# Performance work log

Measured on AMD Instinct MI355X. Metric: run time of the kernel, lower is better.

The kernel has to match this reference:

```python
import jax, jax.numpy as jnp
import numpy as np

NEG_FILL = -1e4  # finite stand-in for -inf so sort/cumsum stay NaN-free


def entmax15(X):
    """1.5-entmax along the last axis (Peters et al. 2019, sort-based exact algorithm)."""
    X = X - jnp.max(X, axis=-1, keepdims=True)
    X = X * 0.5  # alpha=1.5 transform
    Xsrt = -jnp.sort(-X, axis=-1)  # descending sort
    S = X.shape[-1]
    rho = jnp.arange(1, S + 1, dtype=X.dtype)  # 1..S support-size candidates
    mean = jnp.cumsum(Xsrt, axis=-1) / rho
    mean_sq = jnp.cumsum(Xsrt * Xsrt, axis=-1) / rho
    ss = rho * (mean_sq - mean * mean)          # running k*variance
    delta = (1.0 - ss) / rho
    tau = mean - jnp.sqrt(jnp.clip(delta, 0.0, None))
    support_size = jnp.sum(tau <= Xsrt, axis=-1, keepdims=True)
    tau_star = jnp.take_along_axis(tau, support_size - 1, axis=-1)
    return jnp.square(jnp.clip(X - tau_star, 0.0, None))


def setup_inputs() -> dict:
    key = jax.random.key(0)
    k1, k2 = jax.random.split(key)
    B, S = 32768, 2048
    scores = jax.random.normal(k1, (B, S), dtype=jnp.float32)
    mask = jax.random.randint(k2, (B, S), 0, 2, dtype=jnp.int32)
    mask = mask.at[:, 0].set(1)  # guarantee at least one unmasked token per row
    return {"scores": scores, "mask": mask}


def reference(scores, mask):
    # replace_masked_values(scores, mask, -inf) -> entmax15(dim=-1)
    masked_scores = jnp.where(mask.astype(bool), scores, NEG_FILL)
    return entmax15(masked_scores)
```

## Files before the change

### kernel.cpp

```cpp
#include <hip/hip_runtime.h>


#define NEG_FILL (-1.0e4f)

typedef float float2v __attribute__((ext_vector_type(2)));

static constexpr int S_DIM = 2048;
static constexpr int WAVES_PER_BLOCK = 4;
static constexpr int ROWS_PER_WAVE = 8;
static constexpr int ELEMS = S_DIM / 64;
static constexpr int VEC = ELEMS / 4;
static constexpr int VEC2 = ELEMS / 2;

__global__ __launch_bounds__(256) void entmax15_kernel(
    const float* __restrict__ scores,
    const int*   __restrict__ mask,
    float*       __restrict__ out,
    int nrows)
{
    const int lane = threadIdx.x & 63;
    const int wave = threadIdx.x >> 6;
    const int gw   = blockIdx.x * WAVES_PER_BLOCK + wave;
    const int row0 = gw * ROWS_PER_WAVE;
    if (row0 >= nrows) return;

    float4 sreg[VEC];
    int4   mreg[VEC];

    {
        const float4* __restrict__ s = (const float4*)(scores + (size_t)row0 * S_DIM);
        const int4*   __restrict__ m = (const int4*)(mask   + (size_t)row0 * S_DIM);
#pragma unroll
        for (int j = 0; j < VEC; ++j) {
            sreg[j] = s[lane + 64 * j];
            mreg[j] = m[lane + 64 * j];
        }
    }

    const float2v h05   = {0.5f, 0.5f};
    const float2v one2  = {1.0f, 1.0f};
    const float2v zero2 = {0.0f, 0.0f};

#pragma unroll 1
    for (int r = 0; r < ROWS_PER_WAVE; ++r) {
        const int row = row0 + r;
        if (row >= nrows) break;

        float x[ELEMS];
        float rmax = -3.402823466e38f;
#pragma unroll
        for (int j = 0; j < VEC; ++j) {
            const float4 s = sreg[j];
            const int4   m = mreg[j];
            float v0 = m.x ? s.x : NEG_FILL;
            float v1 = m.y ? s.y : NEG_FILL;
            float v2 = m.z ? s.z : NEG_FILL;
            float v3 = m.w ? s.w : NEG_FILL;
            x[4 * j + 0] = v0;
            x[4 * j + 1] = v1;
            x[4 * j + 2] = v2;
            x[4 * j + 3] = v3;
            rmax = fmaxf(rmax, fmaxf(fmaxf(v0, v1), fmaxf(v2, v3)));
        }

        if (r + 1 < ROWS_PER_WAVE && row + 1 < nrows) {
            const float4* __restrict__ sn = (const float4*)(scores + (size_t)(row + 1) * S_DIM);
            const int4*   __restrict__ mn = (const int4*)(mask   + (size_t)(row + 1) * S_DIM);
#pragma unroll
            for (int j = 0; j < VEC; ++j) {
                sreg[j] = sn[lane + 64 * j];
                mreg[j] = mn[lane + 64 * j];
            }
        }

#pragma unroll
        for (int off = 32; off >= 1; off >>= 1)
            rmax = fmaxf(rmax, __shfl_xor(rmax, off, 64));

        const float2v sh2 = {-0.5f * rmax, -0.5f * rmax};
        float2v* xv = (float2v*)x;

        float2v F2 = zero2, G2 = zero2;
        int K = 0;
#pragma unroll
        for (int i = 0; i < VEC2; ++i) {
            float2v t = __builtin_elementwise_fma(xv[i], h05, sh2);
            xv[i] = t;
            float2v d = t + one2;
            float2v y = __builtin_elementwise_max(d, zero2);
            F2 = __builtin_elementwise_fma(y, y, F2);
            G2 = G2 + y;
            K += __popcll(__ballot(d.x > 0.0f));
            K += __popcll(__ballot(d.y > 0.0f));
        }

        float2v FG;
        FG.x = F2.x + F2.y;
        FG.y = G2.x + G2.y;
#pragma unroll
        for (int off = 32; off >= 1; off >>= 1) {
            float2v t;
            t.x = __shfl_xor(FG.x, off, 64);
            t.y = __shfl_xor(FG.y, off, 64);
            FG += t;
        }

        float c     = FG.x - 1.0f;
        float disc  = fmaf(FG.y, FG.y, -(float)K * c);
        float denom = (disc > 0.0f) ? (FG.y + sqrtf(disc)) : (2.0f * FG.y);
        float u     = c / denom;
        float tau   = -1.0f + u;

#pragma unroll 1
        for (int it = 1; it < 16 && fabsf(u) > 2e-7f; ++it) {
            const float2v t2 = {tau, tau};
            F2 = zero2; G2 = zero2; K = 0;
#pragma unroll
            for (int i = 0; i < VEC2; ++i) {
                float2v d = xv[i] - t2;
                float2v y = __builtin_elementwise_max(d, zero2);
                F2 = __builtin_elementwise_fma(y, y, F2);
                G2 = G2 + y;
                K += __popcll(__ballot(d.x > 0.0f));
                K += __popcll(__ballot(d.y > 0.0f));
            }
            FG.x = F2.x + F2.y;
            FG.y = G2.x + G2.y;
#pragma unroll
            for (int off = 32; off >= 1; off >>= 1) {
                float2v t;
                t.x = __shfl_xor(FG.x, off, 64);
                t.y = __shfl_xor(FG.y, off, 64);
                FG += t;
            }
            c     = FG.x - 1.0f;
            disc  = fmaf(FG.y, FG.y, -(float)K * c);
            denom = (disc > 0.0f) ? (FG.y + sqrtf(disc)) : (2.0f * FG.y);
            u     = c / denom;
            tau  += u;
        }

        float4* __restrict__ orow = (float4*)(out + (size_t)row * S_DIM);
        const float2v t2 = {tau, tau};
#pragma unroll
        for (int j = 0; j < VEC; ++j) {
            float2v y0 = __builtin_elementwise_max(xv[2 * j]     - t2, zero2);
            float2v y1 = __builtin_elementwise_max(xv[2 * j + 1] - t2, zero2);
            float2v o0 = y0 * y0;
            float2v o1 = y1 * y1;
            float4 o;
            o.x = o0.x; o.y = o0.y; o.z = o1.x; o.w = o1.y;
            orow[lane + 64 * j] = o;
        }
    }
}

extern "C" void kernel_launch(void* const* d_in, const int* in_sizes, int n_in,
                              void* d_out, int out_size, void* d_ws, size_t ws_size,
                              hipStream_t stream) {
    const float* scores = (const float*)d_in[0];
    const int*   mask   = (const int*)d_in[1];
    float*       out    = (float*)d_out;

    const int nrows = in_sizes[0] / S_DIM;
    const int rows_per_block = WAVES_PER_BLOCK * ROWS_PER_WAVE;
    const int grid = (nrows + rows_per_block - 1) / rows_per_block;

    entmax15_kernel<<<grid, 256, 0, stream>>>(scores, mask, out, nrows);
}
```

Baseline: 604.4 us.

## Prefetch next row via direct global-to-LDS loads instead of register prefetch

Replaces the register-held prefetch of the next row's scores and mask with global_load_lds DMA into a per-wave LDS buffer, with explicit vmcnt/lgkmcnt waits and sched barriers. The aim is to free the 64 VGPRs used for prefetch and so raise occupancy, while keeping loads overlapped with compute. In exchange it adds LDS reads and 64KB of shared memory per block, which caps the number of resident blocks. The manual waitcnt accounting is fragile: the vmcnt(8) wait can also count outstanding output stores.

```diff
diff --git a/kernel.cpp b/kernel.cpp
--- a/kernel.cpp
+++ b/kernel.cpp
@@ -1,4 +1,5 @@
 #include <hip/hip_runtime.h>
+#include <stdint.h>
 
 
 #define NEG_FILL (-1.0e4f)
@@ -11,6 +12,8 @@
 static constexpr int ELEMS = S_DIM / 64;
 static constexpr int VEC = ELEMS / 4;
 static constexpr int VEC2 = ELEMS / 2;
+static constexpr int ROW_BYTES = S_DIM * 4;
+static constexpr int WBUF_BYTES = 2 * ROW_BYTES;
 
 __global__ __launch_bounds__(256) void entmax15_kernel(
     const float* __restrict__ scores,
@@ -18,24 +21,37 @@
     float*       __restrict__ out,
     int nrows)
 {
+    __shared__ char smem[WAVES_PER_BLOCK * WBUF_BYTES];
+
     const int lane = threadIdx.x & 63;
     const int wave = threadIdx.x >> 6;
-    const int gw   = blockIdx.x * WAVES_PER_BLOCK + wave;
-    const int row0 = gw * ROWS_PER_WAVE;
+    const int row0 = (blockIdx.x * WAVES_PER_BLOCK + wave) * ROWS_PER_WAVE;
     if (row0 >= nrows) return;
 
-    float4 sreg[VEC];
-    int4   mreg[VEC];
+    char* wbuf = &smem[wave * WBUF_BYTES];
+    const char* sbase = (const char*)scores;
+    const char* mbase = (const char*)mask;
 
-    {
-        const float4* __restrict__ s = (const float4*)(scores + (size_t)row0 * S_DIM);
-        const int4*   __restrict__ m = (const int4*)(mask   + (size_t)row0 * S_DIM);
+    auto stage = [&](int row) {
+        const char* srow = sbase + (size_t)row * ROW_BYTES;
+        const char* mrow = mbase + (size_t)row * ROW_BYTES;
 #pragma unroll
         for (int j = 0; j < VEC; ++j) {
-            sreg[j] = s[lane + 64 * j];
-            mreg[j] = m[lane + 64 * j];
+            __builtin_amdgcn_global_load_lds(
+                (const __attribute__((address_space(1))) void*)(srow + lane * 16 + j * 1024),
+                (__attribute__((address_space(3))) void*)(wbuf + j * 1024),
+                16, 0, 0);
         }
-    }
+#pragma unroll
+        for (int j = 0; j < VEC; ++j) {
+            __builtin_amdgcn_global_load_lds(
+                (const __attribute__((address_space(1))) void*)(mrow + lane * 16 + j * 1024),
+                (__attribute__((address_space(3))) void*)(wbuf + ROW_BYTES + j * 1024),
+                16, 0, 0);
+        }
+    };
+
+    stage(row0);
 
     const float2v h05   = {0.5f, 0.5f};
     const float2v one2  = {1.0f, 1.0f};
@@ -46,12 +62,21 @@
         const int row = row0 + r;
         if (row >= nrows) break;
 
+        if (r == 0) {
+            asm volatile("s_waitcnt vmcnt(0)" ::: "memory");
+        } else {
+            asm volatile("s_waitcnt vmcnt(8)" ::: "memory");
+        }
+        __builtin_amdgcn_sched_barrier(0);
+
+        const float4* __restrict__ sl = (const float4*)wbuf;
+        const int4*   __restrict__ ml = (const int4*)(wbuf + ROW_BYTES);
         float x[ELEMS];
         float rmax = -3.402823466e38f;
 #pragma unroll
         for (int j = 0; j < VEC; ++j) {
-            const float4 s = sreg[j];
-            const int4   m = mreg[j];
+            const float4 s = sl[64 * j + lane];
+            const int4   m = ml[64 * j + lane];
             float v0 = m.x ? s.x : NEG_FILL;
             float v1 = m.y ? s.y : NEG_FILL;
             float v2 = m.z ? s.z : NEG_FILL;
@@ -62,16 +87,12 @@
             x[4 * j + 3] = v3;
             rmax = fmaxf(rmax, fmaxf(fmaxf(v0, v1), fmaxf(v2, v3)));
         }
+        asm volatile("s_waitcnt lgkmcnt(0)" ::: "memory");
+        __builtin_amdgcn_sched_barrier(0);
 
-        if (r + 1 < ROWS_PER_WAVE && row + 1 < nrows) {
-            const float4* __restrict__ sn = (const float4*)(scores + (size_t)(row + 1) * S_DIM);
-            const int4*   __restrict__ mn = (const int4*)(mask   + (size_t)(row + 1) * S_DIM);
-#pragma unroll
-            for (int j = 0; j < VEC; ++j) {
-                sreg[j] = sn[lane + 64 * j];
-                mreg[j] = mn[lane + 64 * j];
-            }
-        }
+        if (r + 1 < ROWS_PER_WAVE && row + 1 < nrows)
+            stage(row + 1);
+        __builtin_amdgcn_sched_barrier(0);
 
 #pragma unroll
         for (int off = 32; off >= 1; off >>= 1)
@@ -150,7 +171,7 @@
             float2v o1 = y1 * y1;
             float4 o;
             o.x = o0.x; o.y = o0.y; o.z = o1.x; o.w = o1.y;
-            orow[lane + 64 * j] = o;
+            orow[64 * j + lane] = o;
         }
     }
 }
```

Measured after the change: 599.0 us. No clear change (-0.9%).
